# Kernel optimization log

Measured on AMD Instinct MI355X. Metric: run time of the kernel, lower is better.

Reference implementation:

```python
import jax, jax.numpy as jnp
import numpy as np

B, NQ, K = 256, 16, 200           # batch, num_neg+1, num_keys
KEY_SIZE, QUERY_SIZE, HIDDEN = 64, 64, 128
NEG_INF_SCALE = -1000000000.0


def setup_inputs() -> dict:
    key = jax.random.key(0)
    ks = jax.random.split(key, 9)
    queries = jax.random.normal(ks[0], (B, NQ, QUERY_SIZE), dtype=jnp.float32)
    keys = jax.random.normal(ks[1], (B, K, KEY_SIZE), dtype=jnp.float32)
    cum_subs_masks = (jax.random.uniform(ks[2], (B, NQ, K, 1)) < 0.3).astype(jnp.float32)
    s = 1.0 / np.sqrt(HIDDEN)
    Wq = jax.random.normal(ks[3], (QUERY_SIZE, HIDDEN), dtype=jnp.float32) * s
    bq = jnp.zeros((HIDDEN,), dtype=jnp.float32)
    Wk = jax.random.normal(ks[4], (KEY_SIZE, HIDDEN), dtype=jnp.float32) * s
    bk = jnp.zeros((HIDDEN,), dtype=jnp.float32)
    Wv = jax.random.normal(ks[5], (HIDDEN, 1), dtype=jnp.float32) * s
    bv = jnp.zeros((1,), dtype=jnp.float32)
    return {"queries": queries, "keys": keys, "cum_subs_masks": cum_subs_masks,
            "num_neg": NQ - 1, "Wq": Wq, "bq": bq, "Wk": Wk, "bk": bk,
            "Wv": Wv, "bv": bv}


def reference(queries, keys, cum_subs_masks, num_neg, Wq, bq, Wk, bk, Wv, bv):
    # project once, broadcast instead of expanding keys per query (same math)
    qh = queries @ Wq + bq                 # (B, NQ, H)
    kh = keys @ Wk + bk                    # (B, K, H)
    h = jnp.tanh(qh[:, :, None, :] + kh[:, None, :, :])   # (B, NQ, K, H)
    scores = h @ Wv + bv                   # (B, NQ, K, 1)
    if cum_subs_masks is not None:
        scores = scores + cum_subs_masks * NEG_INF_SCALE
    attn_weight = jax.nn.softmax(scores, axis=-2)          # softmax over keys
    attn_out = jnp.sum(attn_weight * keys[:, None, :, :], axis=-2)  # (B, NQ, key_size)
    return (attn_out, attn_weight)
```

## Files before the change

kernel.cpp:

```cpp
#include <hip/hip_runtime.h>
#include <hip/hip_bf16.h>

namespace {

typedef __attribute__((ext_vector_type(8))) short short8;
typedef __attribute__((ext_vector_type(4))) float f32x4;

constexpr int kNB = 256;
constexpr int kNQ = 16;
constexpr int kNK = 200;
constexpr int kDK = 64;
constexpr int kNH = 128;
constexpr int kThreads = 1024;
constexpr int kS = 132;
constexpr float kNeg = -1000000000.0f;
constexpr float kC2 = 2.8853900817779268f;

constexpr int kKhFloats = kNK * kS;
constexpr int kScFloats = kNQ * kNK;
constexpr int kQhFloats = kNQ * kNH;
constexpr size_t kSmemBytes =
    (size_t)(kKhFloats + kScFloats + kQhFloats) * sizeof(float);

__device__ __forceinline__ float exp2_hw(float x) {
#if defined(__has_builtin)
# if __has_builtin(__builtin_amdgcn_exp2f)
  return __builtin_amdgcn_exp2f(x);
# else
  return __expf(x * 0.69314718055994531f);
# endif
#else
  return __expf(x * 0.69314718055994531f);
#endif
}

template <int CTRL>
__device__ __forceinline__ float dpp_add(float v) {
  int sw = __builtin_amdgcn_update_dpp(0, __float_as_int(v), CTRL, 0xF, 0xF, true);
  return v + __int_as_float(sw);
}

__device__ __forceinline__ void split8(float4 a, float4 b, short8& hi, short8& lo) {
  float v[8] = {a.x, a.y, a.z, a.w, b.x, b.y, b.z, b.w};
#pragma unroll
  for (int j = 0; j < 8; ++j) {
    const __hip_bfloat16 h = __float2bfloat16(v[j]);
    hi[j] = (short)__bfloat16_as_ushort(h);
    const __hip_bfloat16 l = __float2bfloat16(v[j] - __bfloat162float(h));
    lo[j] = (short)__bfloat16_as_ushort(l);
  }
}

__launch_bounds__(kThreads)
__attribute__((amdgpu_waves_per_eu(4, 4)))
__global__ void bahdanau_fused(const float* __restrict__ queries,
                               const float* __restrict__ keys,
                               const float* __restrict__ masks,
                               const float* __restrict__ Wq,
                               const float* __restrict__ bq,
                               const float* __restrict__ Wk,
                               const float* __restrict__ bk,
                               const float* __restrict__ Wv,
                               float* __restrict__ out_attn,
                               float* __restrict__ out_w) {
  extern __shared__ __align__(16) float smem[];
  float* skh = smem;
  float* ssc = smem + kKhFloats;
  float* sqh = smem + kKhFloats + kScFloats;

  const int tid  = threadIdx.x;
  const int b    = blockIdx.x;
  const int lane = tid & 63;
  const int wave = __builtin_amdgcn_readfirstlane(tid >> 6);
  const int l15  = lane & 15;
  const int q16  = lane >> 4;
  const int hbase = 8 * l15;

  const float* kb = keys + (size_t)b * kNK * kDK;
  const float* qb = queries + (size_t)b * kNQ * kDK;

  {
    const int tc  = wave >> 1;
    const int odd = wave & 1;
    const int col = tc * 16 + l15;
    const int kj0 = q16 * 8;

    short8 bh[2], bl[2];
#pragma unroll
    for (int p = 0; p < 2; ++p) {
      float4 v0, v1;
      v0.x = Wk[(p * 32 + kj0 + 0) * kNH + col];
      v0.y = Wk[(p * 32 + kj0 + 1) * kNH + col];
      v0.z = Wk[(p * 32 + kj0 + 2) * kNH + col];
      v0.w = Wk[(p * 32 + kj0 + 3) * kNH + col];
      v1.x = Wk[(p * 32 + kj0 + 4) * kNH + col];
      v1.y = Wk[(p * 32 + kj0 + 5) * kNH + col];
      v1.z = Wk[(p * 32 + kj0 + 6) * kNH + col];
      v1.w = Wk[(p * 32 + kj0 + 7) * kNH + col];
      split8(v0, v1, bh[p], bl[p]);
    }
    const float bkc = bk[col];

    const int trB = odd ? 7 : 0;
    const int trE = odd ? 13 : 7;
    for (int tr = trB; tr < trE; ++tr) {
      f32x4 acc = {0.f, 0.f, 0.f, 0.f};
      const int row = tr * 16 + l15;
      const bool ok = row < kNK;
#pragma unroll
      for (int p = 0; p < 2; ++p) {
        float4 a0 = {0.f, 0.f, 0.f, 0.f}, a1 = {0.f, 0.f, 0.f, 0.f};
        if (ok) {
          const float* ap = kb + (size_t)row * kDK + p * 32 + kj0;
          a0 = *reinterpret_cast<const float4*>(ap);
          a1 = *reinterpret_cast<const float4*>(ap + 4);
        }
        short8 ah, al;
        split8(a0, a1, ah, al);
        acc = __builtin_amdgcn_mfma_f32_16x16x32_bf16(al, bh[p], acc, 0, 0, 0);
        acc = __builtin_amdgcn_mfma_f32_16x16x32_bf16(ah, bl[p], acc, 0, 0, 0);
        acc = __builtin_amdgcn_mfma_f32_16x16x32_bf16(ah, bh[p], acc, 0, 0, 0);
      }
#pragma unroll
      for (int r = 0; r < 4; ++r) {
        const int rr = tr * 16 + q16 * 4 + r;
        if (rr < kNK) skh[(size_t)rr * kS + col] = exp2_hw(kC2 * (acc[r] + bkc));
      }
    }

    if (odd) {
      short8 qbh[2], qbl[2];
#pragma unroll
      for (int p = 0; p < 2; ++p) {
        float4 v0, v1;
        v0.x = Wq[(p * 32 + kj0 + 0) * kNH + col];
        v0.y = Wq[(p * 32 + kj0 + 1) * kNH + col];
        v0.z = Wq[(p * 32 + kj0 + 2) * kNH + col];
        v0.w = Wq[(p * 32 + kj0 + 3) * kNH + col];
        v1.x = Wq[(p * 32 + kj0 + 4) * kNH + col];
        v1.y = Wq[(p * 32 + kj0 + 5) * kNH + col];
        v1.z = Wq[(p * 32 + kj0 + 6) * kNH + col];
        v1.w = Wq[(p * 32 + kj0 + 7) * kNH + col];
        split8(v0, v1, qbh[p], qbl[p]);
      }
      const float bqc = bq[col];
      f32x4 acc = {0.f, 0.f, 0.f, 0.f};
#pragma unroll
      for (int p = 0; p < 2; ++p) {
        const float* ap = qb + (size_t)l15 * kDK + p * 32 + kj0;
        const float4 a0 = *reinterpret_cast<const float4*>(ap);
        const float4 a1 = *reinterpret_cast<const float4*>(ap + 4);
        short8 ah, al;
        split8(a0, a1, ah, al);
        acc = __builtin_amdgcn_mfma_f32_16x16x32_bf16(al, qbh[p], acc, 0, 0, 0);
        acc = __builtin_amdgcn_mfma_f32_16x16x32_bf16(ah, qbl[p], acc, 0, 0, 0);
        acc = __builtin_amdgcn_mfma_f32_16x16x32_bf16(ah, qbh[p], acc, 0, 0, 0);
      }
#pragma unroll
      for (int r = 0; r < 4; ++r)
        sqh[(size_t)(q16 * 4 + r) * kNH + col] = exp2_hw(kC2 * (acc[r] + bqc));
    }
  }

  float wv2[8];
  {
    const float4 wva = *reinterpret_cast<const float4*>(&Wv[hbase]);
    const float4 wvb = *reinterpret_cast<const float4*>(&Wv[hbase + 4]);
    wv2[0] = -2.0f * wva.x; wv2[1] = -2.0f * wva.y;
    wv2[2] = -2.0f * wva.z; wv2[3] = -2.0f * wva.w;
    wv2[4] = -2.0f * wvb.x; wv2[5] = -2.0f * wvb.y;
    wv2[6] = -2.0f * wvb.z; wv2[7] = -2.0f * wvb.w;
  }

  __syncthreads();

  const int qg = wave >> 2;
  const int kg = wave & 3;
  float qreg[4][8];
#pragma unroll
  for (int qi = 0; qi < 4; ++qi) {
    const float4 qa  = *reinterpret_cast<const float4*>(&sqh[(4 * qg + qi) * kNH + hbase]);
    const float4 qb4 = *reinterpret_cast<const float4*>(&sqh[(4 * qg + qi) * kNH + hbase + 4]);
    qreg[qi][0] = qa.x;  qreg[qi][1] = qa.y;  qreg[qi][2] = qa.z;  qreg[qi][3] = qa.w;
    qreg[qi][4] = qb4.x; qreg[qi][5] = qb4.y; qreg[qi][6] = qb4.z; qreg[qi][7] = qb4.w;
  }
#pragma unroll
  for (int qi = 0; qi < 4; ++qi)
#pragma unroll
    for (int m = 0; m < 8; ++m) asm volatile("" : "+v"(qreg[qi][m]));

  {
    auto score_k = [&](int k) {
      const float* krow = &skh[(size_t)k * kS + hbase];
      const float4 ka  = *reinterpret_cast<const float4*>(krow);
      const float4 kb4 = *reinterpret_cast<const float4*>(krow + 4);
#pragma unroll
      for (int qi = 0; qi < 4; ++qi) {
        const float uA = fmaf(qreg[qi][0], ka.x, 1.0f);
        const float vA = fmaf(qreg[qi][1], ka.y, 1.0f);
        const float wA = fmaf(qreg[qi][2], ka.z, 1.0f);
        const float xA = fmaf(qreg[qi][3], ka.w, 1.0f);
        const float p1A = uA * vA;
        const float p2A = wA * xA;
        const float n1A = fmaf(wv2[0], vA, wv2[1] * uA);
        const float n2A = fmaf(wv2[2], xA, wv2[3] * wA);
        const float denA = p1A * p2A;
        const float numA = fmaf(n1A, p2A, n2A * p1A);
        const float uB = fmaf(qreg[qi][4], kb4.x, 1.0f);
        const float vB = fmaf(qreg[qi][5], kb4.y, 1.0f);
        const float wB = fmaf(qreg[qi][6], kb4.z, 1.0f);
        const float xB = fmaf(qreg[qi][7], kb4.w, 1.0f);
        const float p1B = uB * vB;
        const float p2B = wB * xB;
        const float n1B = fmaf(wv2[4], vB, wv2[5] * uB);
        const float n2B = fmaf(wv2[6], xB, wv2[7] * wB);
        const float denB = p1B * p2B;
        const float numB = fmaf(n1B, p2B, n2B * p1B);
        const float rA = __builtin_amdgcn_rcpf(denA);
        const float rB = __builtin_amdgcn_rcpf(denB);
        float acc = fmaf(numB, rB, numA * rA);
        acc = dpp_add<0xB1>(acc);
        acc = dpp_add<0x4E>(acc);
        acc = dpp_add<0x141>(acc);
        acc = dpp_add<0x140>(acc);
        if (l15 == 0) ssc[(4 * qg + qi) * kNK + k] = acc;
      }
    };
    for (int i = 0; i < 12; ++i) score_k(16 * i + 4 * kg + q16);
    if (kg < 2) score_k(192 + 4 * kg + q16);
  }

  const float* mrow = masks + ((size_t)b * kNQ + wave) * kNK;
  const bool tail = lane < (kNK - 192);
  const float mm0 = mrow[lane];
  const float mm1 = mrow[lane + 64];
  const float mm2 = mrow[lane + 128];
  const float mm3 = tail ? mrow[lane + 192] : 0.0f;

  __syncthreads();

  {
    const float* sr = &ssc[wave * kNK];
    float v0 = fmaf(mm0, kNeg, sr[lane]);
    float v1 = fmaf(mm1, kNeg, sr[lane + 64]);
    float v2 = fmaf(mm2, kNeg, sr[lane + 128]);
    float v3 = tail ? fmaf(mm3, kNeg, sr[lane + 192]) : -1e30f;
    float m = fmaxf(fmaxf(v0, v1), fmaxf(v2, v3));
#pragma unroll
    for (int off = 32; off > 0; off >>= 1) m = fmaxf(m, __shfl_xor(m, off, 64));
    const float e0 = __expf(v0 - m);
    const float e1 = __expf(v1 - m);
    const float e2 = __expf(v2 - m);
    const float e3 = tail ? __expf(v3 - m) : 0.f;
    float sum = (e0 + e1) + (e2 + e3);
#pragma unroll
    for (int off = 32; off > 0; off >>= 1) sum += __shfl_xor(sum, off, 64);
    const float rs = __builtin_amdgcn_rcpf(sum);
    float* og = out_w + ((size_t)b * kNQ + wave) * kNK;
    float* swr = &ssc[wave * kNK];
    const float w0 = e0 * rs, w1 = e1 * rs, w2 = e2 * rs, w3 = e3 * rs;
    swr[lane]       = w0;  og[lane]       = w0;
    swr[lane + 64]  = w1;  og[lane + 64]  = w1;
    swr[lane + 128] = w2;  og[lane + 128] = w2;
    if (tail) { swr[lane + 192] = w3; og[lane + 192] = w3; }
  }
  __syncthreads();

  {
    float* pk = skh;
    const int kstart = 52 * kg;
    const int kend = (kg == 3) ? kNK : (kstart + 52);
    const float* kb2 = kb + lane;
    float acc[4] = {0.f, 0.f, 0.f, 0.f};
    for (int k0 = kstart; k0 < kend; k0 += 4) {
      const float kv0 = kb2[(size_t)(k0 + 0) * kDK];
      const float kv1 = kb2[(size_t)(k0 + 1) * kDK];
      const float kv2 = kb2[(size_t)(k0 + 2) * kDK];
      const float kv3 = kb2[(size_t)(k0 + 3) * kDK];
#pragma unroll
      for (int qi = 0; qi < 4; ++qi) {
        const float4 wq = *reinterpret_cast<const float4*>(&ssc[(4 * qg + qi) * kNK + k0]);
        acc[qi] = fmaf(wq.x, kv0, acc[qi]);
        acc[qi] = fmaf(wq.y, kv1, acc[qi]);
        acc[qi] = fmaf(wq.z, kv2, acc[qi]);
        acc[qi] = fmaf(wq.w, kv3, acc[qi]);
      }
    }
#pragma unroll
    for (int qi = 0; qi < 4; ++qi)
      pk[((4 * qg + qi) * 4 + kg) * kDK + lane] = acc[qi];
  }
  __syncthreads();

  {
    const float* pk = skh;
    const float r = pk[(wave * 4 + 0) * kDK + lane] + pk[(wave * 4 + 1) * kDK + lane] +
                    pk[(wave * 4 + 2) * kDK + lane] + pk[(wave * 4 + 3) * kDK + lane];
    out_attn[((size_t)b * kNQ + wave) * kDK + lane] = r;
  }
}

}

extern "C" void kernel_launch(void* const* d_in, const int* in_sizes, int n_in,
                              void* d_out, int out_size, void* d_ws, size_t ws_size,
                              hipStream_t stream) {
  const float* queries = (const float*)d_in[0];
  const float* keys    = (const float*)d_in[1];
  const float* masks   = (const float*)d_in[2];
  const float* Wq = (const float*)d_in[4];
  const float* bq = (const float*)d_in[5];
  const float* Wk = (const float*)d_in[6];
  const float* bk = (const float*)d_in[7];
  const float* Wv = (const float*)d_in[8];

  float* out_attn = (float*)d_out;
  float* out_w    = out_attn + (size_t)kNB * kNQ * kDK;

  hipFuncSetAttribute((const void*)bahdanau_fused,
                      hipFuncAttributeMaxDynamicSharedMemorySize, (int)kSmemBytes);
  bahdanau_fused<<<kNB, kThreads, kSmemBytes, stream>>>(queries, keys, masks, Wq, bq,
                                                        Wk, bk, Wv, out_attn, out_w);
}
```

Before: 36.01 us.

## Fuse softmax and weighted key sum per wave, drop two block barriers

Each wave now computes its own query's weighted sum over all 200 keys right after its softmax. It reads its own weights from shared memory, so no cross-wave split with partial sums and reduction is needed, and two __syncthreads plus the partial-sum scratch go away. The mask loads are also moved ahead of the score phase so their global latency overlaps compute. In exchange each wave reads every key row from global memory (4x more key loads per wave than before) with a longer serial loop.

```diff
diff --git a/kernel.cpp b/kernel.cpp
--- a/kernel.cpp
+++ b/kernel.cpp
@@ -171,6 +171,13 @@
     wv2[4] = -2.0f * wvb.x; wv2[5] = -2.0f * wvb.y;
     wv2[6] = -2.0f * wvb.z; wv2[7] = -2.0f * wvb.w;
   }
+
+  const float* mrow = masks + ((size_t)b * kNQ + wave) * kNK;
+  const bool tail = lane < (kNK - 192);
+  const float mm0 = mrow[lane];
+  const float mm1 = mrow[lane + 64];
+  const float mm2 = mrow[lane + 128];
+  const float mm3 = tail ? mrow[lane + 192] : 0.0f;
 
   __syncthreads();
 
@@ -230,21 +237,14 @@
     if (kg < 2) score_k(192 + 4 * kg + q16);
   }
 
-  const float* mrow = masks + ((size_t)b * kNQ + wave) * kNK;
-  const bool tail = lane < (kNK - 192);
-  const float mm0 = mrow[lane];
-  const float mm1 = mrow[lane + 64];
-  const float mm2 = mrow[lane + 128];
-  const float mm3 = tail ? mrow[lane + 192] : 0.0f;
-
   __syncthreads();
 
   {
-    const float* sr = &ssc[wave * kNK];
-    float v0 = fmaf(mm0, kNeg, sr[lane]);
-    float v1 = fmaf(mm1, kNeg, sr[lane + 64]);
-    float v2 = fmaf(mm2, kNeg, sr[lane + 128]);
-    float v3 = tail ? fmaf(mm3, kNeg, sr[lane + 192]) : -1e30f;
+    float* swr = &ssc[wave * kNK];
+    float v0 = fmaf(mm0, kNeg, swr[lane]);
+    float v1 = fmaf(mm1, kNeg, swr[lane + 64]);
+    float v2 = fmaf(mm2, kNeg, swr[lane + 128]);
+    float v3 = tail ? fmaf(mm3, kNeg, swr[lane + 192]) : -1e30f;
     float m = fmaxf(fmaxf(v0, v1), fmaxf(v2, v3));
 #pragma unroll
     for (int off = 32; off > 0; off >>= 1) m = fmaxf(m, __shfl_xor(m, off, 64));
@@ -257,46 +257,23 @@
     for (int off = 32; off > 0; off >>= 1) sum += __shfl_xor(sum, off, 64);
     const float rs = __builtin_amdgcn_rcpf(sum);
     float* og = out_w + ((size_t)b * kNQ + wave) * kNK;
-    float* swr = &ssc[wave * kNK];
     const float w0 = e0 * rs, w1 = e1 * rs, w2 = e2 * rs, w3 = e3 * rs;
     swr[lane]       = w0;  og[lane]       = w0;
     swr[lane + 64]  = w1;  og[lane + 64]  = w1;
     swr[lane + 128] = w2;  og[lane + 128] = w2;
     if (tail) { swr[lane + 192] = w3; og[lane + 192] = w3; }
-  }
-  __syncthreads();
-
-  {
-    float* pk = skh;
-    const int kstart = 52 * kg;
-    const int kend = (kg == 3) ? kNK : (kstart + 52);
+
     const float* kb2 = kb + lane;
-    float acc[4] = {0.f, 0.f, 0.f, 0.f};
-    for (int k0 = kstart; k0 < kend; k0 += 4) {
-      const float kv0 = kb2[(size_t)(k0 + 0) * kDK];
-      const float kv1 = kb2[(size_t)(k0 + 1) * kDK];
-      const float kv2 = kb2[(size_t)(k0 + 2) * kDK];
-      const float kv3 = kb2[(size_t)(k0 + 3) * kDK];
-#pragma unroll
-      for (int qi = 0; qi < 4; ++qi) {
-        const float4 wq = *reinterpret_cast<const float4*>(&ssc[(4 * qg + qi) * kNK + k0]);
-        acc[qi] = fmaf(wq.x, kv0, acc[qi]);
-        acc[qi] = fmaf(wq.y, kv1, acc[qi]);
-        acc[qi] = fmaf(wq.z, kv2, acc[qi]);
-        acc[qi] = fmaf(wq.w, kv3, acc[qi]);
-      }
+    float a0 = 0.f, a1 = 0.f, a2 = 0.f, a3 = 0.f;
+#pragma unroll 2
+    for (int k0 = 0; k0 < kNK; k0 += 4) {
+      const float4 wq = *reinterpret_cast<const float4*>(&swr[k0]);
+      a0 = fmaf(wq.x, kb2[(size_t)(k0 + 0) * kDK], a0);
+      a1 = fmaf(wq.y, kb2[(size_t)(k0 + 1) * kDK], a1);
+      a2 = fmaf(wq.z, kb2[(size_t)(k0 + 2) * kDK], a2);
+      a3 = fmaf(wq.w, kb2[(size_t)(k0 + 3) * kDK], a3);
     }
-#pragma unroll
-    for (int qi = 0; qi < 4; ++qi)
-      pk[((4 * qg + qi) * 4 + kg) * kDK + lane] = acc[qi];
-  }
-  __syncthreads();
-
-  {
-    const float* pk = skh;
-    const float r = pk[(wave * 4 + 0) * kDK + lane] + pk[(wave * 4 + 1) * kDK + lane] +
-                    pk[(wave * 4 + 2) * kDK + lane] + pk[(wave * 4 + 3) * kDK + lane];
-    out_attn[((size_t)b * kNQ + wave) * kDK + lane] = r;
+    out_attn[((size_t)b * kNQ + wave) * kDK + lane] = (a0 + a1) + (a2 + a3);
   }
 }
 
```

New measurement: 39.71 us. 10.3% more time.
